# Optimization experiments

Measured on AMD Instinct MI355X. Metric: run time of the kernel, lower is better.

Reference implementation:

```python
import jax, jax.numpy as jnp
import numpy as np

N = 100000
E = 1600000
IN_DIM = 165
HID = 128
OUT_H = 64  # hidden_dim // 2

def setup_inputs() -> dict:
    key = jax.random.key(0)
    ks = jax.random.split(key, 8)
    x = jax.random.normal(ks[0], (N, IN_DIM), dtype=jnp.float32)
    edge_index = jax.random.randint(ks[1], (2, E), 0, N, dtype=jnp.int64)
    s1 = 1.0 / np.sqrt(IN_DIM)
    s2 = 1.0 / np.sqrt(HID)
    s3 = 1.0 / np.sqrt(OUT_H)
    return {
        "x": x,
        "edge_index": edge_index,
        "W1": jax.random.normal(ks[2], (IN_DIM, HID), dtype=jnp.float32) * s1,
        "b1": jnp.zeros((HID,), jnp.float32),
        "Wg": jax.random.normal(ks[3], (HID, OUT_H), dtype=jnp.float32) * s2,
        "a_src": jax.random.normal(ks[4], (OUT_H,), dtype=jnp.float32) * s3,
        "a_dst": jax.random.normal(ks[5], (OUT_H,), dtype=jnp.float32) * s3,
        "bg": jnp.zeros((OUT_H,), jnp.float32),
        "Wfc": jax.random.normal(ks[6], (OUT_H, 2), dtype=jnp.float32) * s3,
        "bfc": jnp.zeros((2,), jnp.float32),
    }

def _add_self_loops(edge_index, n):
    loops = jnp.arange(n, dtype=edge_index.dtype)
    row = jnp.concatenate([edge_index[0], loops])
    col = jnpp_concat = jnp.concatenate([edge_index[1], loops])
    return row, col

def _gcn_layer(x, row, col, W, b, n):
    deg = jax.ops.segment_sum(jnp.ones_like(col, dtype=x.dtype), col, num_segments=n)
    dinv = jnp.where(deg > 0, jax.lax.rsqrt(deg), 0.0)
    h = x @ W                                   # [N, HID]
    msg = h[row] * (dinv[row] * dinv[col])[:, None]  # [E+N, HID]
    return jax.ops.segment_sum(msg, col, num_segments=n) + b

def _gat_layer(x, row, col, W, a_src, a_dst, b, n):
    # single-head GATConv with self-loops, LeakyReLU(0.2), segment softmax over dst
    h = x @ W                                   # [N, OUT_H]
    e = jax.nn.leaky_relu((h @ a_src)[row] + (h @ a_dst)[col], negative_slope=0.2)
    m = jax.ops.segment_max(e, col, num_segments=n)
    ex = jnp.exp(e - m[col])
    s = jax.ops.segment_sum(ex, col, num_segments=n)
    alpha = ex / s[col]                         # every node has a self-loop => s > 0
    out = jax.ops.segment_sum(alpha[:, None] * h[row], col, num_segments=n)
    return out + b

def reference(x, edge_index, W1, b1, Wg, a_src, a_dst, bg, Wfc, bfc):
    n = x.shape[0]
    row, col = _add_self_loops(edge_index, n)
    h = jax.nn.relu(_gcn_layer(x, row, col, W1, b1, n))
    h = jax.nn.relu(_gat_layer(h, row, col, Wg, a_src, a_dst, bg, n))
    return h @ Wfc + bfc
```

## Files before the change

### kernel.cpp

```cpp
#include <hip/hip_runtime.h>
#include <math.h>

#define NSL 0.2f
#define IN_DIM 165
#define HID 128
#define OUT_H 64
#define SCAN_B 512
#define NCB_MAX 512
#define EPB 4096

typedef __attribute__((ext_vector_type(8))) short bf16x8;
typedef __attribute__((ext_vector_type(4))) float f32x4;

__device__ inline unsigned pack_bf16(float a, float b) {
    unsigned ua = __float_as_uint(a);
    ua += 0x7FFFu + ((ua >> 16) & 1u);
    unsigned ub = __float_as_uint(b);
    ub += 0x7FFFu + ((ub >> 16) & 1u);
    return (ua >> 16) | (ub & 0xFFFF0000u);
}

__device__ __host__ inline int pcol(int i) {
    int j = i >> 1, odd = i & 1;
    return 32 * (j >> 4) + (j & 15) + 16 * odd;
}

__global__ __launch_bounds__(256) void chist(const int* __restrict__ coli, int E,
                                             int* __restrict__ ghist, int ncb) {
    __shared__ int h[NCB_MAX];
    for (int i = threadIdx.x; i < ncb; i += 256) h[i] = 0;
    __syncthreads();
    int e0 = blockIdx.x * EPB;
    int e1 = min(e0 + EPB, E);
    for (int e = e0 + threadIdx.x; e < e1; e += 256)
        atomicAdd(&h[coli[e] >> 8], 1);
    __syncthreads();
    for (int i = threadIdx.x; i < ncb; i += 256)
        if (h[i]) atomicAdd(&ghist[i], h[i]);
}

__global__ __launch_bounds__(NCB_MAX) void cscan(const int* __restrict__ ghist,
                                                 int* __restrict__ cstart,
                                                 int* __restrict__ gcursor,
                                                 int ncb, int E) {
    __shared__ int tmp[NCB_MAX];
    int tid = threadIdx.x;
    int v = (tid < ncb) ? ghist[tid] : 0;
    tmp[tid] = v;
    __syncthreads();
    for (int off = 1; off < NCB_MAX; off <<= 1) {
        int t = (tid >= off) ? tmp[tid - off] : 0;
        __syncthreads();
        tmp[tid] += t;
        __syncthreads();
    }
    if (tid < ncb) {
        int excl = tmp[tid] - v;
        cstart[tid] = excl;
        gcursor[tid] = excl;
    }
    if (tid == ncb - 1) cstart[ncb] = E;
}

__global__ __launch_bounds__(256) void pass1_scatter(const int* __restrict__ rowi,
                                                     const int* __restrict__ coli, int E,
                                                     int* __restrict__ gcursor,
                                                     unsigned* __restrict__ ebuf, int ncb) {
    __shared__ int hist[NCB_MAX];
    __shared__ int base[NCB_MAX];
    int e0 = blockIdx.x * EPB;
    int e1 = min(e0 + EPB, E);
    for (int i = threadIdx.x; i < ncb; i += 256) hist[i] = 0;
    __syncthreads();
    for (int e = e0 + threadIdx.x; e < e1; e += 256)
        atomicAdd(&hist[coli[e] >> 8], 1);
    __syncthreads();
    for (int i = threadIdx.x; i < ncb; i += 256) {
        int h = hist[i];
        base[i] = h ? atomicAdd(&gcursor[i], h) : 0;
        hist[i] = 0;
    }
    __syncthreads();
    for (int e = e0 + threadIdx.x; e < e1; e += 256) {
        int c = coli[e];
        int cb = c >> 8;
        int rank = atomicAdd(&hist[cb], 1);
        ebuf[base[cb] + rank] = ((unsigned)rowi[e] << 8) | (unsigned)(c & 255);
    }
}

__global__ __launch_bounds__(256) void pass2_count(const unsigned* __restrict__ ebuf,
                                                   const int* __restrict__ cstart,
                                                   int* __restrict__ degi, int n) {
    __shared__ int cnt[256];
    int cb = blockIdx.x;
    cnt[threadIdx.x] = 0;
    __syncthreads();
    int s = cstart[cb], e1 = cstart[cb + 1];
    for (int e = s + threadIdx.x; e < e1; e += 256)
        atomicAdd(&cnt[ebuf[e] & 255u], 1);
    __syncthreads();
    int node = (cb << 8) + threadIdx.x;
    if (node < n) degi[node] = cnt[threadIdx.x];
}

__global__ __launch_bounds__(SCAN_B) void scan_block(const int* __restrict__ degi,
                                                     int* __restrict__ incl,
                                                     int* __restrict__ bsums, int n) {
    __shared__ int tmp[SCAN_B];
    int tid = threadIdx.x;
    int gid = blockIdx.x * SCAN_B + tid;
    int v = (gid < n) ? degi[gid] : 0;
    tmp[tid] = v;
    __syncthreads();
    for (int off = 1; off < SCAN_B; off <<= 1) {
        int t = (tid >= off) ? tmp[tid - off] : 0;
        __syncthreads();
        tmp[tid] += t;
        __syncthreads();
    }
    if (gid < n) incl[gid] = tmp[tid];
    if (tid == SCAN_B - 1) bsums[blockIdx.x] = tmp[tid];
}

__global__ __launch_bounds__(256) void scan_bsums(int* __restrict__ bsums, int nb) {
    __shared__ int tmp[256];
    int tid = threadIdx.x;
    int v = (tid < nb) ? bsums[tid] : 0;
    tmp[tid] = v;
    __syncthreads();
    for (int off = 1; off < 256; off <<= 1) {
        int t = (tid >= off) ? tmp[tid - off] : 0;
        __syncthreads();
        tmp[tid] += t;
        __syncthreads();
    }
    if (tid < nb) bsums[tid] = tmp[tid] - v;
}

__global__ __launch_bounds__(256) void scan_finalize(const int* __restrict__ degi,
                                                     const int* __restrict__ bsums,
                                                     int* __restrict__ offsets,
                                                     float* __restrict__ dinv,
                                                     int n, int E) {
    int gid = blockIdx.x * 256 + threadIdx.x;
    if (gid < n) {
        int excl = offsets[gid] - degi[gid] + bsums[gid >> 9];
        offsets[gid] = excl;
        dinv[gid] = rsqrtf((float)degi[gid] + 1.0f);
    } else if (gid == n) {
        offsets[n] = E;
    }
}

__global__ __launch_bounds__(256) void pass2_fill(const unsigned* __restrict__ ebuf,
                                                  const int* __restrict__ cstart,
                                                  const int* __restrict__ offsets,
                                                  int* __restrict__ csr_src, int n) {
    __shared__ int cnt[256];
    __shared__ int offs[256];
    int cb = blockIdx.x;
    int node = (cb << 8) + threadIdx.x;
    cnt[threadIdx.x] = 0;
    offs[threadIdx.x] = (node < n) ? offsets[node] : 0;
    __syncthreads();
    int s = cstart[cb], e1 = cstart[cb + 1];
    for (int e = s + threadIdx.x; e < e1; e += 256) {
        unsigned v = ebuf[e];
        int local = v & 255u;
        int rank = atomicAdd(&cnt[local], 1);
        csr_src[offs[local] + rank] = (int)(v >> 8);
    }
}

__global__ __launch_bounds__(256) void wprep(const float* __restrict__ W1,
                                             const float* __restrict__ b1,
                                             uint4* __restrict__ wfrag,
                                             float* __restrict__ b1p) {
    int idx = blockIdx.x * 256 + threadIdx.x;
    if (idx < 3072) {
        int q = idx & 3, n = (idx >> 2) & 127, c = idx >> 9;
        int k0 = c * 32 + q * 8;
        float f[8];
#pragma unroll
        for (int j = 0; j < 8; j++) {
            int k = k0 + j;
            f[j] = (k < IN_DIM) ? W1[k * 128 + n] : 0.f;
        }
        uint4 u;
        u.x = pack_bf16(f[0], f[1]);
        u.y = pack_bf16(f[2], f[3]);
        u.z = pack_bf16(f[4], f[5]);
        u.w = pack_bf16(f[6], f[7]);
        wfrag[idx] = u;
    }
    if (blockIdx.x == 0 && threadIdx.x < 128) b1p[threadIdx.x] = b1[pcol(threadIdx.x)];
}

__global__ __launch_bounds__(256) void wprep2(const float* __restrict__ Wg,
                                              const float* __restrict__ bg,
                                              const float* __restrict__ Wfc,
                                              uint4* __restrict__ wg2frag,
                                              float* __restrict__ bgp,
                                              float2* __restrict__ wfcp) {
    int idx = blockIdx.x * 256 + threadIdx.x;
    if (idx < 1024) {
        int q = idx & 3, n = (idx >> 2) & 63, c = idx >> 8;
        float f[8];
#pragma unroll
        for (int j = 0; j < 8; j++) {
            int ks = c * 32 + q * 8 + j;
            f[j] = Wg[pcol(ks) * 64 + n];
        }
        uint4 u;
        u.x = pack_bf16(f[0], f[1]);
        u.y = pack_bf16(f[2], f[3]);
        u.z = pack_bf16(f[4], f[5]);
        u.w = pack_bf16(f[6], f[7]);
        wg2frag[idx] = u;
    }
    if (blockIdx.x == 0 && threadIdx.x < 64) {
        int i = threadIdx.x;
        int o = pcol(i);
        bgp[i] = bg[o];
        wfcp[i] = make_float2(Wfc[o * 2], Wfc[o * 2 + 1]);
    }
}

__global__ __launch_bounds__(256) void xprep(const float* __restrict__ x,
                                             unsigned* __restrict__ xb, int N) {
    int tid = blockIdx.x * 256 + threadIdx.x;
    if (tid >= N * 24) return;
    int row = tid / 24, seg = tid % 24;
    int k0 = seg * 8;
    const float* xr = x + (size_t)row * IN_DIM + k0;
    float f[8];
#pragma unroll
    for (int j = 0; j < 8; j++)
        f[j] = (k0 + j < IN_DIM) ? xr[j] : 0.f;
    uint4 u;
    u.x = pack_bf16(f[0], f[1]);
    u.y = pack_bf16(f[2], f[3]);
    u.z = pack_bf16(f[4], f[5]);
    u.w = pack_bf16(f[6], f[7]);
    *(uint4*)&xb[(size_t)row * 96 + seg * 4] = u;
}

__global__ __launch_bounds__(256) void gemm1_mfma(const uint4* __restrict__ xb,
                                                  const uint4* __restrict__ wfrag,
                                                  const float* __restrict__ dinv,
                                                  unsigned* __restrict__ h1p, int M) {
    const int t = threadIdx.x;
    const int wave = t >> 6;
    const int lane = t & 63;
    const int l16 = lane & 15;
    const int quad = lane >> 4;
    const int rowbase = blockIdx.x * 64 + wave * 16;

    int arow = rowbase + l16;
    if (arow >= M) arow = M - 1;

    f32x4 acc[8];
#pragma unroll
    for (int nt = 0; nt < 8; nt++) acc[nt] = (f32x4){0.f, 0.f, 0.f, 0.f};

#pragma unroll
    for (int c = 0; c < 6; c++) {
        uint4 au = xb[(size_t)arow * 24 + c * 4 + quad];
        bf16x8 a = __builtin_bit_cast(bf16x8, au);
#pragma unroll
        for (int nt = 0; nt < 8; nt++) {
            uint4 bu = wfrag[(size_t)((c * 128 + nt * 16 + l16) * 4 + quad)];
            bf16x8 b = __builtin_bit_cast(bf16x8, bu);
            acc[nt] = __builtin_amdgcn_mfma_f32_16x16x32_bf16(a, b, acc[nt], 0, 0, 0);
        }
    }

#pragma unroll
    for (int r = 0; r < 4; r++) {
        int row = rowbase + quad * 4 + r;
        if (row < M) {
            float s = dinv[row];
#pragma unroll
            for (int p = 0; p < 4; p++) {
                h1p[(size_t)row * 64 + p * 16 + l16] =
                    pack_bf16(acc[2 * p][r] * s, acc[2 * p + 1][r] * s);
            }
        }
    }
}

__device__ inline void acc8(float* a, uint4 u) {
    a[0] += __uint_as_float(u.x << 16);
    a[1] += __uint_as_float(u.x & 0xFFFF0000u);
    a[2] += __uint_as_float(u.y << 16);
    a[3] += __uint_as_float(u.y & 0xFFFF0000u);
    a[4] += __uint_as_float(u.z << 16);
    a[5] += __uint_as_float(u.z & 0xFFFF0000u);
    a[6] += __uint_as_float(u.w << 16);
    a[7] += __uint_as_float(u.w & 0xFFFF0000u);
}

__device__ inline void fma8(float* a, uint4 u, float w) {
    a[0] = fmaf(__uint_as_float(u.x << 16), w, a[0]);
    a[1] = fmaf(__uint_as_float(u.x & 0xFFFF0000u), w, a[1]);
    a[2] = fmaf(__uint_as_float(u.y << 16), w, a[2]);
    a[3] = fmaf(__uint_as_float(u.y & 0xFFFF0000u), w, a[3]);
    a[4] = fmaf(__uint_as_float(u.z << 16), w, a[4]);
    a[5] = fmaf(__uint_as_float(u.z & 0xFFFF0000u), w, a[5]);
    a[6] = fmaf(__uint_as_float(u.w << 16), w, a[6]);
    a[7] = fmaf(__uint_as_float(u.w & 0xFFFF0000u), w, a[7]);
}

__global__ __launch_bounds__(256) void gcn_gather(const int* __restrict__ offsets,
                                                  const int* __restrict__ csr_src,
                                                  const uint4* __restrict__ h1v,
                                                  const float* __restrict__ dinv,
                                                  const float* __restrict__ b1p,
                                                  uint4* __restrict__ gb, int n) {
    int node = (blockIdx.x * 256 + threadIdx.x) >> 4;
    int lane = threadIdx.x & 15;
    if (node >= n) return;
    int s0 = offsets[node], s1 = offsets[node + 1];

    float a0[8], a1[8], a2[8], a3[8];
#pragma unroll
    for (int i = 0; i < 8; i++) { a0[i] = 0.f; a1[i] = 0.f; a2[i] = 0.f; a3[i] = 0.f; }
    acc8(a0, h1v[(size_t)node * 16 + lane]);

    int k = s0;
    for (; k + 4 <= s1; k += 4) {
        int r0 = csr_src[k], r1 = csr_src[k + 1], r2 = csr_src[k + 2], r3 = csr_src[k + 3];
        uint4 v0 = h1v[(size_t)r0 * 16 + lane];
        uint4 v1 = h1v[(size_t)r1 * 16 + lane];
        uint4 v2 = h1v[(size_t)r2 * 16 + lane];
        uint4 v3 = h1v[(size_t)r3 * 16 + lane];
        acc8(a0, v0);
        acc8(a1, v1);
        acc8(a2, v2);
        acc8(a3, v3);
    }
    for (; k < s1; k++) {
        int r = csr_src[k];
        acc8(a0, h1v[(size_t)r * 16 + lane]);
    }

    float dc = dinv[node];
    float4 bb0 = ((const float4*)b1p)[lane * 2];
    float4 bb1 = ((const float4*)b1p)[lane * 2 + 1];
    float o[8];
    o[0] = fmaxf(((a0[0] + a1[0]) + (a2[0] + a3[0])) * dc + bb0.x, 0.f);
    o[1] = fmaxf(((a0[1] + a1[1]) + (a2[1] + a3[1])) * dc + bb0.y, 0.f);
    o[2] = fmaxf(((a0[2] + a1[2]) + (a2[2] + a3[2])) * dc + bb0.z, 0.f);
    o[3] = fmaxf(((a0[3] + a1[3]) + (a2[3] + a3[3])) * dc + bb0.w, 0.f);
    o[4] = fmaxf(((a0[4] + a1[4]) + (a2[4] + a3[4])) * dc + bb1.x, 0.f);
    o[5] = fmaxf(((a0[5] + a1[5]) + (a2[5] + a3[5])) * dc + bb1.y, 0.f);
    o[6] = fmaxf(((a0[6] + a1[6]) + (a2[6] + a3[6])) * dc + bb1.z, 0.f);
    o[7] = fmaxf(((a0[7] + a1[7]) + (a2[7] + a3[7])) * dc + bb1.w, 0.f);
    uint4 pk;
    pk.x = pack_bf16(o[0], o[1]);
    pk.y = pack_bf16(o[2], o[3]);
    pk.z = pack_bf16(o[4], o[5]);
    pk.w = pack_bf16(o[6], o[7]);
    gb[(size_t)node * 16 + lane] = pk;
}

__global__ __launch_bounds__(256) void gemm2_mfma(const uint4* __restrict__ gb4,
                                                  const uint4* __restrict__ wg2frag,
                                                  const float* __restrict__ a_src,
                                                  const float* __restrict__ a_dst,
                                                  unsigned* __restrict__ h2b,
                                                  float* __restrict__ es,
                                                  float* __restrict__ ed, int M) {
    const int t = threadIdx.x;
    const int wave = t >> 6;
    const int lane = t & 63;
    const int l16 = lane & 15;
    const int quad = lane >> 4;
    const int rowbase = blockIdx.x * 64 + wave * 16;

    int arow = rowbase + l16;
    if (arow >= M) arow = M - 1;

    f32x4 acc[4];
#pragma unroll
    for (int nt = 0; nt < 4; nt++) acc[nt] = (f32x4){0.f, 0.f, 0.f, 0.f};

#pragma unroll
    for (int c = 0; c < 4; c++) {
        uint4 au = gb4[(size_t)arow * 16 + c * 4 + quad];
        bf16x8 a = __builtin_bit_cast(bf16x8, au);
#pragma unroll
        for (int nt = 0; nt < 4; nt++) {
            uint4 bu = wg2frag[(size_t)((c * 64 + nt * 16 + l16) * 4 + quad)];
            bf16x8 b = __builtin_bit_cast(bf16x8, bu);
            acc[nt] = __builtin_amdgcn_mfma_f32_16x16x32_bf16(a, b, acc[nt], 0, 0, 0);
        }
    }

    float as0 = a_src[l16], as1 = a_src[16 + l16], as2 = a_src[32 + l16], as3 = a_src[48 + l16];
    float ad0 = a_dst[l16], ad1 = a_dst[16 + l16], ad2 = a_dst[32 + l16], ad3 = a_dst[48 + l16];

#pragma unroll
    for (int r = 0; r < 4; r++) {
        int row = rowbase + quad * 4 + r;
        float ps = acc[0][r] * as0 + acc[1][r] * as1 + acc[2][r] * as2 + acc[3][r] * as3;
        float pd = acc[0][r] * ad0 + acc[1][r] * ad1 + acc[2][r] * ad2 + acc[3][r] * ad3;
#pragma unroll
        for (int m = 8; m; m >>= 1) {
            ps += __shfl_xor(ps, m, 16);
            pd += __shfl_xor(pd, m, 16);
        }
        if (row < M) {
            h2b[(size_t)row * 32 + l16]      = pack_bf16(acc[0][r], acc[1][r]);
            h2b[(size_t)row * 32 + 16 + l16] = pack_bf16(acc[2][r], acc[3][r]);
            if (l16 == 0) { es[row] = ps; ed[row] = pd; }
        }
    }
}

__global__ __launch_bounds__(256) void gat_fused(const int* __restrict__ offsets,
                                                 const int* __restrict__ csr_src,
                                                 const uint4* __restrict__ h2v,
                                                 const float* __restrict__ es,
                                                 const float* __restrict__ ed,
                                                 const float* __restrict__ bgp,
                                                 const float2* __restrict__ wfcp,
                                                 const float* __restrict__ bfc,
                                                 float* __restrict__ out, int n) {
    int node = (blockIdx.x * 256 + threadIdx.x) >> 3;
    int lane = threadIdx.x & 7;
    if (node >= n) return;
    int s0 = offsets[node], s1 = offsets[node + 1];
    float edc = ed[node];

    float eself = es[node] + edc;
    eself = eself > 0.f ? eself : NSL * eself;
    float x0s = __expf(eself);
    float sA = x0s, sB = 0.f, sC = 0.f, sD = 0.f;
    float aA[8], aB[8], aC[8], aD[8];
#pragma unroll
    for (int i = 0; i < 8; i++) { aA[i] = 0.f; aB[i] = 0.f; aC[i] = 0.f; aD[i] = 0.f; }
    fma8(aA, h2v[(size_t)node * 8 + lane], x0s);

    int k = s0;
    for (; k + 4 <= s1; k += 4) {
        int r0 = csr_src[k], r1 = csr_src[k + 1], r2 = csr_src[k + 2], r3 = csr_src[k + 3];
        float e0 = es[r0] + edc, e1 = es[r1] + edc, e2 = es[r2] + edc, e3 = es[r3] + edc;
        e0 = e0 > 0.f ? e0 : NSL * e0;
        e1 = e1 > 0.f ? e1 : NSL * e1;
        e2 = e2 > 0.f ? e2 : NSL * e2;
        e3 = e3 > 0.f ? e3 : NSL * e3;
        float x0 = __expf(e0), x1 = __expf(e1), x2 = __expf(e2), x3 = __expf(e3);
        uint4 v0 = h2v[(size_t)r0 * 8 + lane];
        uint4 v1 = h2v[(size_t)r1 * 8 + lane];
        uint4 v2 = h2v[(size_t)r2 * 8 + lane];
        uint4 v3 = h2v[(size_t)r3 * 8 + lane];
        sA += x0; sB += x1; sC += x2; sD += x3;
        fma8(aA, v0, x0);
        fma8(aB, v1, x1);
        fma8(aC, v2, x2);
        fma8(aD, v3, x3);
    }
    for (; k < s1; k++) {
        int r = csr_src[k];
        float e = es[r] + edc;
        e = e > 0.f ? e : NSL * e;
        float xv = __expf(e);
        sA += xv;
        fma8(aA, h2v[(size_t)r * 8 + lane], xv);
    }
    float s = (sA + sB) + (sC + sD);
    float rcp = 1.0f / s;
    float4 b0 = ((const float4*)bgp)[lane * 2];
    float4 b1 = ((const float4*)bgp)[lane * 2 + 1];
    float o[8];
    o[0] = fmaxf(((aA[0] + aB[0]) + (aC[0] + aD[0])) * rcp + b0.x, 0.f);
    o[1] = fmaxf(((aA[1] + aB[1]) + (aC[1] + aD[1])) * rcp + b0.y, 0.f);
    o[2] = fmaxf(((aA[2] + aB[2]) + (aC[2] + aD[2])) * rcp + b0.z, 0.f);
    o[3] = fmaxf(((aA[3] + aB[3]) + (aC[3] + aD[3])) * rcp + b0.w, 0.f);
    o[4] = fmaxf(((aA[4] + aB[4]) + (aC[4] + aD[4])) * rcp + b1.x, 0.f);
    o[5] = fmaxf(((aA[5] + aB[5]) + (aC[5] + aD[5])) * rcp + b1.y, 0.f);
    o[6] = fmaxf(((aA[6] + aB[6]) + (aC[6] + aD[6])) * rcp + b1.z, 0.f);
    o[7] = fmaxf(((aA[7] + aB[7]) + (aC[7] + aD[7])) * rcp + b1.w, 0.f);

    float p0 = 0.f, p1 = 0.f;
#pragma unroll
    for (int m2 = 0; m2 < 4; m2++) {
        float4 w = ((const float4*)wfcp)[lane * 4 + m2];
        p0 += o[2 * m2] * w.x + o[2 * m2 + 1] * w.z;
        p1 += o[2 * m2] * w.y + o[2 * m2 + 1] * w.w;
    }
#pragma unroll
    for (int m = 4; m; m >>= 1) {
        p0 += __shfl_xor(p0, m, 8);
        p1 += __shfl_xor(p1, m, 8);
    }
    if (lane == 0) {
        out[(size_t)node * 2 + 0] = p0 + bfc[0];
        out[(size_t)node * 2 + 1] = p1 + bfc[1];
    }
}

extern "C" void kernel_launch(void* const* d_in, const int* in_sizes, int n_in,
                              void* d_out, int out_size, void* d_ws, size_t ws_size,
                              hipStream_t stream) {
    const float* x     = (const float*)d_in[0];
    const int*   ei    = (const int*)d_in[1];
    const float* W1    = (const float*)d_in[2];
    const float* b1    = (const float*)d_in[3];
    const float* Wg    = (const float*)d_in[4];
    const float* a_src = (const float*)d_in[5];
    const float* a_dst = (const float*)d_in[6];
    const float* bg    = (const float*)d_in[7];
    const float* Wfc   = (const float*)d_in[8];
    const float* bfc   = (const float*)d_in[9];
    float* out = (float*)d_out;

    const int N = in_sizes[0] / IN_DIM;
    const int E = in_sizes[1] / 2;
    const int* rowi = ei;
    const int* coli = ei + E;
    const int ncb = (N + 255) >> 8;

    auto alignup = [](char* p) { return (char*)(((uintptr_t)p + 15) & ~(uintptr_t)15); };

    char* wsb = (char*)d_ws;
    int*   degi    = (int*)wsb;
    int*   offsets = degi + N;
    float* dinv    = (float*)(offsets + N + 8);
    float* es      = dinv + N;
    float* ed      = es + N;
    int*   ghist   = (int*)(ed + N);
    int*   cstart  = ghist + NCB_MAX;
    int*   gcursor = cstart + NCB_MAX + 2;
    int*   bsums   = gcursor + NCB_MAX;
    float* b1p     = (float*)(bsums + 512);
    float* bgp     = b1p + 128;
    float2* wfcp   = (float2*)(bgp + 64);
    uint4* wfrag   = (uint4*)alignup((char*)(wfcp + 64));
    uint4* wg2frag = wfrag + 3072;
    int*   csr_src = (int*)(wg2frag + 1024);
    unsigned* ebuf = (unsigned*)(csr_src + E);
    unsigned* h1p  = (unsigned*)alignup((char*)(ebuf + E));
    unsigned* xgb  = (unsigned*)alignup((char*)(h1p + (size_t)N * 64));
    unsigned* xb   = xgb;
    uint4* gb      = (uint4*)xgb;
    unsigned* h2b  = h1p;

    hipMemsetAsync(ghist, 0, NCB_MAX * 4, stream);

    const int nbE = (E + EPB - 1) / EPB;
    const int nbScan = (N + SCAN_B - 1) / SCAN_B;

    chist<<<nbE, 256, 0, stream>>>(coli, E, ghist, ncb);
    cscan<<<1, NCB_MAX, 0, stream>>>(ghist, cstart, gcursor, ncb, E);
    pass1_scatter<<<nbE, 256, 0, stream>>>(rowi, coli, E, gcursor, ebuf, ncb);
    pass2_count<<<ncb, 256, 0, stream>>>(ebuf, cstart, degi, N);
    scan_block<<<nbScan, SCAN_B, 0, stream>>>(degi, offsets, bsums, N);
    scan_bsums<<<1, 256, 0, stream>>>(bsums, nbScan);
    scan_finalize<<<(N + 256) / 256, 256, 0, stream>>>(degi, bsums, offsets, dinv, N, E);
    pass2_fill<<<ncb, 256, 0, stream>>>(ebuf, cstart, offsets, csr_src, N);

    wprep<<<12, 256, 0, stream>>>(W1, b1, wfrag, b1p);
    wprep2<<<4, 256, 0, stream>>>(Wg, bg, Wfc, wg2frag, bgp, wfcp);
    xprep<<<(N * 24 + 255) / 256, 256, 0, stream>>>(x, xb, N);

    gemm1_mfma<<<(N + 63) / 64, 256, 0, stream>>>((const uint4*)xb, wfrag, dinv, h1p, N);

    gcn_gather<<<(N + 15) / 16, 256, 0, stream>>>(offsets, csr_src, (const uint4*)h1p,
                                                  dinv, b1p, gb, N);

    gemm2_mfma<<<(N + 63) / 64, 256, 0, stream>>>(gb, wg2frag, a_src, a_dst, h2b, es, ed, N);

    gat_fused<<<(N + 31) / 32, 256, 0, stream>>>(offsets, csr_src, (const uint4*)h2b,
                                                 es, ed, bgp, wfcp, bfc, out, N);
}
```

Measured before the change: 387.1 us.

## Fuse CSR degree count, scan and fill; fold x bf16 conversion into GEMM1

Merges pass2_count, the three-kernel global scan and pass2_fill into one per-column-bucket kernel. Because edges are already bucketed by column block, the local prefix over 256 nodes plus cstart gives global offsets directly. Also merges the two weight-prep kernels into one launch and removes the xprep pass by having gemm1 read fp32 x and pack to bf16 on the fly. This cuts several launches and avoids writing and re-reading the bf16 x copy, at the cost of unaligned fp32 loads of x inside the GEMM.

```diff
diff --git a/kernel.cpp b/kernel.cpp
--- a/kernel.cpp
+++ b/kernel.cpp
@@ -5,7 +5,6 @@
 #define IN_DIM 165
 #define HID 128
 #define OUT_H 64
-#define SCAN_B 512
 #define NCB_MAX 512
 #define EPB 4096
 
@@ -89,94 +88,61 @@
     }
 }
 
-__global__ __launch_bounds__(256) void pass2_count(const unsigned* __restrict__ ebuf,
-                                                   const int* __restrict__ cstart,
-                                                   int* __restrict__ degi, int n) {
+__global__ __launch_bounds__(256) void pass2_all(const unsigned* __restrict__ ebuf,
+                                                 const int* __restrict__ cstart,
+                                                 int* __restrict__ offsets,
+                                                 float* __restrict__ dinv,
+                                                 int* __restrict__ csr_src,
+                                                 int n, int E) {
     __shared__ int cnt[256];
-    int cb = blockIdx.x;
-    cnt[threadIdx.x] = 0;
+    __shared__ int scan[256];
+    __shared__ int offs[256];
+    const int tid = threadIdx.x;
+    const int cb = blockIdx.x;
+    cnt[tid] = 0;
     __syncthreads();
     int s = cstart[cb], e1 = cstart[cb + 1];
-    for (int e = s + threadIdx.x; e < e1; e += 256)
+    for (int e = s + tid; e < e1; e += 256)
         atomicAdd(&cnt[ebuf[e] & 255u], 1);
     __syncthreads();
-    int node = (cb << 8) + threadIdx.x;
-    if (node < n) degi[node] = cnt[threadIdx.x];
-}
-
-__global__ __launch_bounds__(SCAN_B) void scan_block(const int* __restrict__ degi,
-                                                     int* __restrict__ incl,
-                                                     int* __restrict__ bsums, int n) {
-    __shared__ int tmp[SCAN_B];
-    int tid = threadIdx.x;
-    int gid = blockIdx.x * SCAN_B + tid;
-    int v = (gid < n) ? degi[gid] : 0;
-    tmp[tid] = v;
-    __syncthreads();
-    for (int off = 1; off < SCAN_B; off <<= 1) {
-        int t = (tid >= off) ? tmp[tid - off] : 0;
+    int v = cnt[tid];
+    scan[tid] = v;
+    __syncthreads();
+#pragma unroll
+    for (int off = 1; off < 256; off <<= 1) {
+        int t = (tid >= off) ? scan[tid - off] : 0;
         __syncthreads();
-        tmp[tid] += t;
+        scan[tid] += t;
         __syncthreads();
     }
-    if (gid < n) incl[gid] = tmp[tid];
-    if (tid == SCAN_B - 1) bsums[blockIdx.x] = tmp[tid];
-}
-
-__global__ __launch_bounds__(256) void scan_bsums(int* __restrict__ bsums, int nb) {
-    __shared__ int tmp[256];
-    int tid = threadIdx.x;
-    int v = (tid < nb) ? bsums[tid] : 0;
-    tmp[tid] = v;
-    __syncthreads();
-    for (int off = 1; off < 256; off <<= 1) {
-        int t = (tid >= off) ? tmp[tid - off] : 0;
-        __syncthreads();
-        tmp[tid] += t;
-        __syncthreads();
-    }
-    if (tid < nb) bsums[tid] = tmp[tid] - v;
-}
-
-__global__ __launch_bounds__(256) void scan_finalize(const int* __restrict__ degi,
-                                                     const int* __restrict__ bsums,
-                                                     int* __restrict__ offsets,
-                                                     float* __restrict__ dinv,
-                                                     int n, int E) {
-    int gid = blockIdx.x * 256 + threadIdx.x;
-    if (gid < n) {
-        int excl = offsets[gid] - degi[gid] + bsums[gid >> 9];
-        offsets[gid] = excl;
-        dinv[gid] = rsqrtf((float)degi[gid] + 1.0f);
-    } else if (gid == n) {
-        offsets[n] = E;
-    }
-}
-
-__global__ __launch_bounds__(256) void pass2_fill(const unsigned* __restrict__ ebuf,
-                                                  const int* __restrict__ cstart,
-                                                  const int* __restrict__ offsets,
-                                                  int* __restrict__ csr_src, int n) {
-    __shared__ int cnt[256];
-    __shared__ int offs[256];
-    int cb = blockIdx.x;
-    int node = (cb << 8) + threadIdx.x;
-    cnt[threadIdx.x] = 0;
-    offs[threadIdx.x] = (node < n) ? offsets[node] : 0;
-    __syncthreads();
-    int s = cstart[cb], e1 = cstart[cb + 1];
-    for (int e = s + threadIdx.x; e < e1; e += 256) {
-        unsigned v = ebuf[e];
-        int local = v & 255u;
+    int off0 = s + scan[tid] - v;
+    offs[tid] = off0;
+    int node = (cb << 8) + tid;
+    if (node < n) {
+        offsets[node] = off0;
+        dinv[node] = rsqrtf((float)v + 1.0f);
+    }
+    if (cb == 0 && tid == 0) offsets[n] = E;
+    cnt[tid] = 0;
+    __syncthreads();
+    for (int e = s + tid; e < e1; e += 256) {
+        unsigned u = ebuf[e];
+        int local = u & 255u;
         int rank = atomicAdd(&cnt[local], 1);
-        csr_src[offs[local] + rank] = (int)(v >> 8);
-    }
-}
-
-__global__ __launch_bounds__(256) void wprep(const float* __restrict__ W1,
-                                             const float* __restrict__ b1,
-                                             uint4* __restrict__ wfrag,
-                                             float* __restrict__ b1p) {
+        csr_src[offs[local] + rank] = (int)(u >> 8);
+    }
+}
+
+__global__ __launch_bounds__(256) void wprep_all(const float* __restrict__ W1,
+                                                 const float* __restrict__ b1,
+                                                 const float* __restrict__ Wg,
+                                                 const float* __restrict__ bg,
+                                                 const float* __restrict__ Wfc,
+                                                 uint4* __restrict__ wfrag,
+                                                 float* __restrict__ b1p,
+                                                 uint4* __restrict__ wg2frag,
+                                                 float* __restrict__ bgp,
+                                                 float2* __restrict__ wfcp) {
     int idx = blockIdx.x * 256 + threadIdx.x;
     if (idx < 3072) {
         int q = idx & 3, n = (idx >> 2) & 127, c = idx >> 9;
@@ -193,19 +159,9 @@
         u.z = pack_bf16(f[4], f[5]);
         u.w = pack_bf16(f[6], f[7]);
         wfrag[idx] = u;
-    }
-    if (blockIdx.x == 0 && threadIdx.x < 128) b1p[threadIdx.x] = b1[pcol(threadIdx.x)];
-}
-
-__global__ __launch_bounds__(256) void wprep2(const float* __restrict__ Wg,
-                                              const float* __restrict__ bg,
-                                              const float* __restrict__ Wfc,
-                                              uint4* __restrict__ wg2frag,
-                                              float* __restrict__ bgp,
-                                              float2* __restrict__ wfcp) {
-    int idx = blockIdx.x * 256 + threadIdx.x;
-    if (idx < 1024) {
-        int q = idx & 3, n = (idx >> 2) & 63, c = idx >> 8;
+    } else if (idx < 4096) {
+        int i2 = idx - 3072;
+        int q = i2 & 3, n = (i2 >> 2) & 63, c = i2 >> 8;
         float f[8];
 #pragma unroll
         for (int j = 0; j < 8; j++) {
@@ -217,36 +173,17 @@
         u.y = pack_bf16(f[2], f[3]);
         u.z = pack_bf16(f[4], f[5]);
         u.w = pack_bf16(f[6], f[7]);
-        wg2frag[idx] = u;
-    }
-    if (blockIdx.x == 0 && threadIdx.x < 64) {
-        int i = threadIdx.x;
-        int o = pcol(i);
-        bgp[i] = bg[o];
-        wfcp[i] = make_float2(Wfc[o * 2], Wfc[o * 2 + 1]);
-    }
-}
-
-__global__ __launch_bounds__(256) void xprep(const float* __restrict__ x,
-                                             unsigned* __restrict__ xb, int N) {
-    int tid = blockIdx.x * 256 + threadIdx.x;
-    if (tid >= N * 24) return;
-    int row = tid / 24, seg = tid % 24;
-    int k0 = seg * 8;
-    const float* xr = x + (size_t)row * IN_DIM + k0;
-    float f[8];
-#pragma unroll
-    for (int j = 0; j < 8; j++)
-        f[j] = (k0 + j < IN_DIM) ? xr[j] : 0.f;
-    uint4 u;
-    u.x = pack_bf16(f[0], f[1]);
-    u.y = pack_bf16(f[2], f[3]);
-    u.z = pack_bf16(f[4], f[5]);
-    u.w = pack_bf16(f[6], f[7]);
-    *(uint4*)&xb[(size_t)row * 96 + seg * 4] = u;
-}
-
-__global__ __launch_bounds__(256) void gemm1_mfma(const uint4* __restrict__ xb,
+        wg2frag[i2] = u;
+    }
+    if (idx < 128) b1p[idx] = b1[pcol(idx)];
+    if (idx < 64) {
+        int o = pcol(idx);
+        bgp[idx] = bg[o];
+        wfcp[idx] = make_float2(Wfc[o * 2], Wfc[o * 2 + 1]);
+    }
+}
+
+__global__ __launch_bounds__(256) void gemm1_mfma(const float* __restrict__ x,
                                                   const uint4* __restrict__ wfrag,
                                                   const float* __restrict__ dinv,
                                                   unsigned* __restrict__ h1p, int M) {
@@ -259,6 +196,7 @@
 
     int arow = rowbase + l16;
     if (arow >= M) arow = M - 1;
+    const float* xr = x + (size_t)arow * IN_DIM;
 
     f32x4 acc[8];
 #pragma unroll
@@ -266,7 +204,16 @@
 
 #pragma unroll
     for (int c = 0; c < 6; c++) {
-        uint4 au = xb[(size_t)arow * 24 + c * 4 + quad];
+        int k0 = c * 32 + quad * 8;
+        float f[8];
+#pragma unroll
+        for (int j = 0; j < 8; j++)
+            f[j] = (k0 + j < IN_DIM) ? xr[k0 + j] : 0.f;
+        uint4 au;
+        au.x = pack_bf16(f[0], f[1]);
+        au.y = pack_bf16(f[2], f[3]);
+        au.z = pack_bf16(f[4], f[5]);
+        au.w = pack_bf16(f[6], f[7]);
         bf16x8 a = __builtin_bit_cast(bf16x8, au);
 #pragma unroll
         for (int nt = 0; nt < 8; nt++) {
@@ -526,16 +473,14 @@
     auto alignup = [](char* p) { return (char*)(((uintptr_t)p + 15) & ~(uintptr_t)15); };
 
     char* wsb = (char*)d_ws;
-    int*   degi    = (int*)wsb;
-    int*   offsets = degi + N;
+    int*   offsets = (int*)wsb;
     float* dinv    = (float*)(offsets + N + 8);
     float* es      = dinv + N;
     float* ed      = es + N;
     int*   ghist   = (int*)(ed + N);
     int*   cstart  = ghist + NCB_MAX;
     int*   gcursor = cstart + NCB_MAX + 2;
-    int*   bsums   = gcursor + NCB_MAX;
-    float* b1p     = (float*)(bsums + 512);
+    float* b1p     = (float*)(gcursor + NCB_MAX);
     float* bgp     = b1p + 128;
     float2* wfcp   = (float2*)(bgp + 64);
     uint4* wfrag   = (uint4*)alignup((char*)(wfcp + 64));
@@ -543,30 +488,21 @@
     int*   csr_src = (int*)(wg2frag + 1024);
     unsigned* ebuf = (unsigned*)(csr_src + E);
     unsigned* h1p  = (unsigned*)alignup((char*)(ebuf + E));
-    unsigned* xgb  = (unsigned*)alignup((char*)(h1p + (size_t)N * 64));
-    unsigned* xb   = xgb;
-    uint4* gb      = (uint4*)xgb;
+    uint4* gb      = (uint4*)alignup((char*)(h1p + (size_t)N * 64));
     unsigned* h2b  = h1p;
 
     hipMemsetAsync(ghist, 0, NCB_MAX * 4, stream);
 
     const int nbE = (E + EPB - 1) / EPB;
-    const int nbScan = (N + SCAN_B - 1) / SCAN_B;
 
     chist<<<nbE, 256, 0, stream>>>(coli, E, ghist, ncb);
     cscan<<<1, NCB_MAX, 0, stream>>>(ghist, cstart, gcursor, ncb, E);
     pass1_scatter<<<nbE, 256, 0, stream>>>(rowi, coli, E, gcursor, ebuf, ncb);
-    pass2_count<<<ncb, 256, 0, stream>>>(ebuf, cstart, degi, N);
-    scan_block<<<nbScan, SCAN_B, 0, stream>>>(degi, offsets, bsums, N);
-    scan_bsums<<<1, 256, 0, stream>>>(bsums, nbScan);
-    scan_finalize<<<(N + 256) / 256, 256, 0, stream>>>(degi, bsums, offsets, dinv, N, E);
-    pass2_fill<<<ncb, 256, 0, stream>>>(ebuf, cstart, offsets, csr_src, N);
-
-    wprep<<<12, 256, 0, stream>>>(W1, b1, wfrag, b1p);
-    wprep2<<<4, 256, 0, stream>>>(Wg, bg, Wfc, wg2frag, bgp, wfcp);
-    xprep<<<(N * 24 + 255) / 256, 256, 0, stream>>>(x, xb, N);
-
-    gemm1_mfma<<<(N + 63) / 64, 256, 0, stream>>>((const uint4*)xb, wfrag, dinv, h1p, N);
+    pass2_all<<<ncb, 256, 0, stream>>>(ebuf, cstart, offsets, dinv, csr_src, N, E);
+
+    wprep_all<<<16, 256, 0, stream>>>(W1, b1, Wg, bg, Wfc, wfrag, b1p, wg2frag, bgp, wfcp);
+
+    gemm1_mfma<<<(N + 63) / 64, 256, 0, stream>>>(x, wfrag, dinv, h1p, N);
 
     gcn_gather<<<(N + 15) / 16, 256, 0, stream>>>(offsets, csr_src, (const uint4*)h1p,
                                                   dinv, b1p, gb, N);
```

Measured after the change: 352.8 us. 8.9% less time.
